# Optimization experiments

Measured on AMD Instinct MI355X. Metric: run time of the kernel, lower is better.

## Reference

```python
import jax, jax.numpy as jnp
import numpy as np

V = 1_000_000
VD = 256
GD = 256
H = 16
G = 50_000
HID = 128


def setup_inputs() -> dict:
    key = jax.random.key(0)
    k1, k2, k3, k4, k5, k6 = jax.random.split(key, 6)
    node_embeddings = jax.random.normal(k1, (V, VD), dtype=jnp.float32)
    node_to_graph_map = jnp.sort(jax.random.randint(k2, (V,), 0, G, dtype=jnp.int32))
    # MLP params (no biases): scoring 256->128->16, transformation 256->128->256
    s = 1.0 / np.sqrt(VD)
    sh = 1.0 / np.sqrt(HID)
    scoring_w1 = jax.random.uniform(k3, (VD, HID), jnp.float32, -s, s)
    scoring_w2 = jax.random.uniform(k4, (HID, H), jnp.float32, -sh, sh)
    transform_w1 = jax.random.uniform(k5, (VD, HID), jnp.float32, -s, s)
    transform_w2 = jax.random.uniform(k6, (HID, GD), jnp.float32, -sh, sh)
    return {
        "node_embeddings": node_embeddings,
        "node_to_graph_map": node_to_graph_map,
        "num_graphs": G,
        "scoring_w1": scoring_w1,
        "scoring_w2": scoring_w2,
        "transform_w1": transform_w1,
        "transform_w2": transform_w2,
    }


def reference(node_embeddings, node_to_graph_map, num_graphs,
              scoring_w1, scoring_w2, transform_w1, transform_w2):
    seg = node_to_graph_map  # [V]
    # Scoring MLP: [V, VD] -> [V, H]
    scores = jax.nn.relu(node_embeddings @ scoring_w1) @ scoring_w2
    # Unsorted segment softmax per head (numerically stable)
    seg_max = jax.ops.segment_max(scores, seg, num_segments=num_graphs)  # [G, H]
    ex = jnp.exp(scores - seg_max[seg])  # [V, H]
    denom = jax.ops.segment_sum(ex, seg, num_segments=num_graphs)  # [G, H]
    weights = ex / denom[seg]  # [V, H]
    # Transformation MLP followed by the extra outer activation in forward()
    node_reprs = jax.nn.relu(jax.nn.relu(node_embeddings @ transform_w1) @ transform_w2)  # [V, GD]
    node_reprs = node_reprs.reshape(-1, H, GD // H)  # [V, H, GD/H]
    weighted = (weights[:, :, None] * node_reprs).reshape(-1, GD)  # [V, GD]
    graph_reprs = jax.ops.segment_sum(weighted, seg, num_segments=num_graphs)  # [G, GD]
    return graph_reprs
```

## Files before the change

kernel.cpp:

```cpp
#include <hip/hip_runtime.h>
#include <stdint.h>

#define VN   1000000
#define VDIM 256
#define GDIM 256
#define NH   16
#define NG   50000
#define HIDD 128
#define NTILES 15625

using bf16x8 = __attribute__((ext_vector_type(8))) __bf16;
using f32x4  = __attribute__((ext_vector_type(4))) float;
using u16x4  = __attribute__((ext_vector_type(4))) unsigned short;

__device__ __forceinline__ unsigned short f2bf(float f) {
  unsigned u = __float_as_uint(f);
  return (unsigned short)((u + 0x7FFFu + ((u >> 16) & 1u)) >> 16);
}
__device__ __forceinline__ f32x4 fzero4() { f32x4 z = {0.f, 0.f, 0.f, 0.f}; return z; }

__global__ void k_prep(const float* __restrict__ s1, const float* __restrict__ s2,
                       const float* __restrict__ t1, const float* __restrict__ t2,
                       unsigned short* __restrict__ WB) {
  int t = blockIdx.x * 256 + threadIdx.x;
  const float* W; unsigned short* dst; int K, N, lid;
  if (t < 32768)       { W = s1; dst = WB;          K = 256; N = 128; lid = t; }
  else if (t < 65536)  { W = t1; dst = WB + 32768;  K = 256; N = 128; lid = t - 32768; }
  else if (t < 98304)  { W = t2; dst = WB + 65536;  K = 128; N = 256; lid = t - 65536; }
  else if (t < 100352) { W = s2; dst = WB + 98304;  K = 128; N = 16;  lid = t - 98304; }
  else return;
  int j = lid & 7, l = (lid >> 3) & 63, rem = lid >> 9;
  int KS = K >> 5;
  int s = rem % KS, c = rem / KS;
  int row = 32 * s + 8 * (l >> 4) + j;
  int col = 16 * c + (l & 15);
  dst[lid] = f2bf(W[row * N + col]);
}

__global__ void k_zero(float* __restrict__ out, float* __restrict__ denom) {
  int i = blockIdx.x * 256 + threadIdx.x;
  float4 z = make_float4(0.f, 0.f, 0.f, 0.f);
  if (i < NG * GDIM / 4) ((float4*)out)[i] = z;
  int j = i - NG * GDIM / 4;
  if (j >= 0 && j < NG * NH / 4) ((float4*)denom)[j] = z;
}

__global__ __launch_bounds__(256, 4) void k_main(
    const float* __restrict__ X,
    const unsigned short* __restrict__ WBs1,
    const unsigned short* __restrict__ WBt1,
    const unsigned short* __restrict__ WBs2,
    const unsigned short* __restrict__ WBt2,
    const int* __restrict__ seg,
    float* __restrict__ denom,
    float* __restrict__ out) {
  __shared__ __align__(16) char U[36864];
  char* const Xs = U;
  char* const Hs = U;
  char* const Ts = U + 16384;
  float* const exs = (float*)(U + 32768);

  const int tid  = threadIdx.x;
  const int lane = tid & 63;
  const int w    = tid >> 6;
  const int lg   = lane >> 4;
  const size_t base = (size_t)blockIdx.x * 64;

  const int gv = seg[base + lane];
  const int gp = __shfl_up(gv, 1, 64);
  const unsigned long long bmask = __ballot(gv != gp) | 1ull;

  {
    const float4* Xg = (const float4*)(X + base * VDIM);
    #pragma unroll
    for (int i = 0; i < 16; ++i) {
      int f = tid + 256 * i;
      int row = f >> 6, c4 = f & 63;
      float4 v = Xg[f];
      u16x4 b = { f2bf(v.x), f2bf(v.y), f2bf(v.z), f2bf(v.w) };
      *(u16x4*)(Xs + row * 512 + ((c4 * 8) ^ ((row & 7) << 4))) = b;
    }
  }
  __syncthreads();

  {
    const unsigned short* WB = (w < 2) ? WBs1 : WBt1;
    const int cbase = (w & 1) * 4;
    f32x4 acc[4][4];
    #pragma unroll
    for (int r = 0; r < 4; ++r)
      #pragma unroll
      for (int c = 0; c < 4; ++c) acc[r][c] = fzero4();

    #pragma unroll
    for (int ks = 0; ks < 8; ++ks) {
      bf16x8 A[4];
      #pragma unroll
      for (int r = 0; r < 4; ++r) {
        int row = 16 * r + (lane & 15);
        int cb = 64 * ks + 16 * (lane >> 4);
        A[r] = *(const bf16x8*)(Xs + row * 512 + (cb ^ ((row & 7) << 4)));
      }
      #pragma unroll
      for (int ci = 0; ci < 4; ++ci) {
        bf16x8 B = *(const bf16x8*)(WB + (size_t)(((cbase + ci) * 8 + ks) * 64 + lane) * 8);
        #pragma unroll
        for (int r = 0; r < 4; ++r)
          acc[r][ci] = __builtin_amdgcn_mfma_f32_16x16x32_bf16(A[r], B, acc[r][ci], 0, 0, 0);
      }
    }
    __syncthreads();

    char* const dst = (w < 2) ? Hs : Ts;
    #pragma unroll
    for (int ci = 0; ci < 4; ++ci) {
      int colf = cbase + ci;
      #pragma unroll
      for (int r = 0; r < 4; ++r) {
        #pragma unroll
        for (int j = 0; j < 4; ++j) {
          int row = 16 * r + 4 * (lane >> 4) + j;
          int col = 16 * colf + (lane & 15);
          float v = acc[r][ci][j];
          v = v > 0.f ? v : 0.f;
          *(unsigned short*)(dst + row * 256 + ((col * 2) ^ ((row & 7) << 4))) = f2bf(v);
        }
      }
    }
  }
  __syncthreads();

  {
    f32x4 sa = fzero4();
    #pragma unroll
    for (int ks = 0; ks < 4; ++ks) {
      int row = 16 * w + (lane & 15);
      int cb = 64 * ks + 16 * (lane >> 4);
      bf16x8 A2 = *(const bf16x8*)(Hs + row * 256 + (cb ^ ((row & 7) << 4)));
      bf16x8 B2 = *(const bf16x8*)(WBs2 + (size_t)(ks * 64 + lane) * 8);
      sa = __builtin_amdgcn_mfma_f32_16x16x32_bf16(A2, B2, sa, 0, 0, 0);
    }
    const int h = lane & 15;
    const int rowbase = 16 * w + 4 * lg;
    float ex[4]; int gs[4];
    #pragma unroll
    for (int j = 0; j < 4; ++j) {
      ex[j] = __expf(sa[j]);
      gs[j] = __shfl(gv, rowbase + j, 64);
      exs[(rowbase + j) * 16 + h] = ex[j];
    }
    float accd = ex[0]; int gcur = gs[0];
    #pragma unroll
    for (int j = 1; j < 4; ++j) {
      if (gs[j] == gcur) accd += ex[j];
      else { atomicAdd(denom + (size_t)gcur * NH + h, accd); gcur = gs[j]; accd = ex[j]; }
    }
    atomicAdd(denom + (size_t)gcur * NH + h, accd);
  }

  f32x4 racc[4][4];
  #pragma unroll
  for (int r = 0; r < 4; ++r)
    #pragma unroll
    for (int c = 0; c < 4; ++c) racc[r][c] = fzero4();
  #pragma unroll
  for (int ks = 0; ks < 4; ++ks) {
    bf16x8 A[4];
    #pragma unroll
    for (int r = 0; r < 4; ++r) {
      int row = 16 * r + (lane & 15);
      int cbyte = 64 * ks + 16 * (lane >> 4);
      A[r] = *(const bf16x8*)(Ts + row * 256 + (cbyte ^ ((row & 7) << 4)));
    }
    #pragma unroll
    for (int ci = 0; ci < 4; ++ci) {
      bf16x8 B = *(const bf16x8*)(WBt2 + (size_t)(((4 * w + ci) * 4 + ks) * 64 + lane) * 8);
      #pragma unroll
      for (int r = 0; r < 4; ++r)
        racc[r][ci] = __builtin_amdgcn_mfma_f32_16x16x32_bf16(A[r], B, racc[r][ci], 0, 0, 0);
    }
  }
  __syncthreads();

  #pragma unroll
  for (int r = 0; r < 4; ++r)
    #pragma unroll
    for (int j = 0; j < 4; ++j) {
      int row = 16 * r + 4 * lg + j;
      f32x4 wr = *(const f32x4*)(exs + row * 16 + 4 * w);
      #pragma unroll
      for (int ci = 0; ci < 4; ++ci) {
        float v = racc[r][ci][j];
        v = v > 0.f ? v : 0.f;
        racc[r][ci][j] = v * wr[ci];
      }
    }

  unsigned long long m = bmask;
  while (m) {
    int a = __builtin_ctzll(m);
    m &= m - 1;
    int b = m ? __builtin_ctzll(m) : 64;
    int g = __shfl(gv, a, 64);
    f32x4 s = fzero4();
    #pragma unroll
    for (int r = 0; r < 4; ++r)
      #pragma unroll
      for (int j = 0; j < 4; ++j) {
        int row = 16 * r + 4 * lg + j;
        float msk = ((unsigned)(row - a) < (unsigned)(b - a)) ? 1.f : 0.f;
        #pragma unroll
        for (int ci = 0; ci < 4; ++ci) s[ci] = fmaf(msk, racc[r][ci][j], s[ci]);
      }
    #pragma unroll
    for (int ci = 0; ci < 4; ++ci) {
      s[ci] += __shfl_xor(s[ci], 16, 64);
      s[ci] += __shfl_xor(s[ci], 32, 64);
    }
    bool edge = (a == 0) || (b == 64);
    if (lane < 16) {
      float* dst = out + (size_t)g * GDIM + 64 * w + lane;
      if (edge) {
        atomicAdd(dst,      s[0]); atomicAdd(dst + 16, s[1]);
        atomicAdd(dst + 32, s[2]); atomicAdd(dst + 48, s[3]);
      } else {
        dst[0] = s[0]; dst[16] = s[1]; dst[32] = s[2]; dst[48] = s[3];
      }
    }
  }
}

__global__ void k_div(float* __restrict__ out, const float* __restrict__ denom) {
  int i = blockIdx.x * 256 + threadIdx.x;
  if (i >= NG * GDIM / 4) return;
  float d = denom[(size_t)(i >> 6) * NH + ((i & 63) >> 2)];
  float r = d > 0.f ? 1.0f / d : 0.f;
  float4 v = ((float4*)out)[i];
  v.x *= r; v.y *= r; v.z *= r; v.w *= r;
  ((float4*)out)[i] = v;
}

extern "C" void kernel_launch(void* const* d_in, const int* in_sizes, int n_in,
                              void* d_out, int out_size, void* d_ws, size_t ws_size,
                              hipStream_t stream) {
  (void)in_sizes; (void)n_in; (void)out_size; (void)ws_size;
  const float* X  = (const float*)d_in[0];
  const int* seg  = (const int*)d_in[1];
  const float* s1 = (const float*)d_in[3];
  const float* s2 = (const float*)d_in[4];
  const float* t1 = (const float*)d_in[5];
  const float* t2 = (const float*)d_in[6];
  float* out = (float*)d_out;
  char* ws = (char*)d_ws;

  unsigned short* WB = (unsigned short*)ws;
  float* denom = (float*)(ws + (1 << 19));

  k_prep<<<392, 256, 0, stream>>>(s1, s2, t1, t2, WB);
  k_zero<<<13282, 256, 0, stream>>>(out, denom);
  k_main<<<NTILES, 256, 0, stream>>>(X, WB, WB + 32768, WB + 98304, WB + 65536,
                                     seg, denom, out);
  k_div<<<12500, 256, 0, stream>>>(out, denom);
}
```

Before: 492.5 us.

## Load X directly from global into MFMA operands, skipping LDS staging

```diff
diff --git a/kernel.cpp b/kernel.cpp
--- a/kernel.cpp
+++ b/kernel.cpp
@@ -14,8 +14,14 @@
 using u16x4  = __attribute__((ext_vector_type(4))) unsigned short;
 
 __device__ __forceinline__ unsigned short f2bf(float f) {
-  unsigned u = __float_as_uint(f);
-  return (unsigned short)((u + 0x7FFFu + ((u >> 16) & 1u)) >> 16);
+  __bf16 h = (__bf16)f;
+  return __builtin_bit_cast(unsigned short, h);
+}
+__device__ __forceinline__ bf16x8 pack8(float4 a, float4 b) {
+  bf16x8 r;
+  r[0] = (__bf16)a.x; r[1] = (__bf16)a.y; r[2] = (__bf16)a.z; r[3] = (__bf16)a.w;
+  r[4] = (__bf16)b.x; r[5] = (__bf16)b.y; r[6] = (__bf16)b.z; r[7] = (__bf16)b.w;
+  return r;
 }
 __device__ __forceinline__ f32x4 fzero4() { f32x4 z = {0.f, 0.f, 0.f, 0.f}; return z; }
 
@@ -55,7 +61,6 @@
     float* __restrict__ denom,
     float* __restrict__ out) {
   __shared__ __align__(16) char U[36864];
-  char* const Xs = U;
   char* const Hs = U;
   char* const Ts = U + 16384;
   float* const exs = (float*)(U + 32768);
@@ -71,21 +76,14 @@
   const unsigned long long bmask = __ballot(gv != gp) | 1ull;
 
   {
-    const float4* Xg = (const float4*)(X + base * VDIM);
-    #pragma unroll
-    for (int i = 0; i < 16; ++i) {
-      int f = tid + 256 * i;
-      int row = f >> 6, c4 = f & 63;
-      float4 v = Xg[f];
-      u16x4 b = { f2bf(v.x), f2bf(v.y), f2bf(v.z), f2bf(v.w) };
-      *(u16x4*)(Xs + row * 512 + ((c4 * 8) ^ ((row & 7) << 4))) = b;
-    }
-  }
-  __syncthreads();
-
-  {
     const unsigned short* WB = (w < 2) ? WBs1 : WBt1;
     const int cbase = (w & 1) * 4;
+    const int m = lane & 15;
+    const float* xp0 = X + (base + m)      * VDIM + 8 * lg;
+    const float* xp1 = xp0 + 16 * VDIM;
+    const float* xp2 = xp1 + 16 * VDIM;
+    const float* xp3 = xp2 + 16 * VDIM;
+
     f32x4 acc[4][4];
     #pragma unroll
     for (int r = 0; r < 4; ++r)
@@ -95,11 +93,15 @@
     #pragma unroll
     for (int ks = 0; ks < 8; ++ks) {
       bf16x8 A[4];
-      #pragma unroll
-      for (int r = 0; r < 4; ++r) {
-        int row = 16 * r + (lane & 15);
-        int cb = 64 * ks + 16 * (lane >> 4);
-        A[r] = *(const bf16x8*)(Xs + row * 512 + (cb ^ ((row & 7) << 4)));
+      {
+        const float4* p0 = (const float4*)(xp0 + 32 * ks);
+        const float4* p1 = (const float4*)(xp1 + 32 * ks);
+        const float4* p2 = (const float4*)(xp2 + 32 * ks);
+        const float4* p3 = (const float4*)(xp3 + 32 * ks);
+        A[0] = pack8(p0[0], p0[1]);
+        A[1] = pack8(p1[0], p1[1]);
+        A[2] = pack8(p2[0], p2[1]);
+        A[3] = pack8(p3[0], p3[1]);
       }
       #pragma unroll
       for (int ci = 0; ci < 4; ++ci) {
@@ -109,7 +111,6 @@
           acc[r][ci] = __builtin_amdgcn_mfma_f32_16x16x32_bf16(A[r], B, acc[r][ci], 0, 0, 0);
       }
     }
-    __syncthreads();
 
     char* const dst = (w < 2) ? Hs : Ts;
     #pragma unroll
@@ -119,8 +120,8 @@
       for (int r = 0; r < 4; ++r) {
         #pragma unroll
         for (int j = 0; j < 4; ++j) {
-          int row = 16 * r + 4 * (lane >> 4) + j;
-          int col = 16 * colf + (lane & 15);
+          int row = 16 * r + 4 * lg + j;
+          int col = 16 * colf + m;
           float v = acc[r][ci][j];
           v = v > 0.f ? v : 0.f;
           *(unsigned short*)(dst + row * 256 + ((col * 2) ^ ((row & 7) << 4))) = f2bf(v);
@@ -135,7 +136,7 @@
     #pragma unroll
     for (int ks = 0; ks < 4; ++ks) {
       int row = 16 * w + (lane & 15);
-      int cb = 64 * ks + 16 * (lane >> 4);
+      int cb = 64 * ks + 16 * lg;
       bf16x8 A2 = *(const bf16x8*)(Hs + row * 256 + (cb ^ ((row & 7) << 4)));
       bf16x8 B2 = *(const bf16x8*)(WBs2 + (size_t)(ks * 64 + lane) * 8);
       sa = __builtin_amdgcn_mfma_f32_16x16x32_bf16(A2, B2, sa, 0, 0, 0);
@@ -169,7 +170,7 @@
     #pragma unroll
     for (int r = 0; r < 4; ++r) {
       int row = 16 * r + (lane & 15);
-      int cbyte = 64 * ks + 16 * (lane >> 4);
+      int cbyte = 64 * ks + 16 * lg;
       A[r] = *(const bf16x8*)(Ts + row * 256 + (cbyte ^ ((row & 7) << 4)));
     }
     #pragma unroll
```

Measured after the change: 740.4 us. 50.3% more time.
